# Kernel tuning notes

Hardware: AMD Instinct MI355X
Metric: run time of the kernel (lower is better)

Reference implementation:

```python
import jax, jax.numpy as jnp
import numpy as np
import math

D_MODEL = 64
H = 8
DK = D_MODEL // H


def setup_inputs() -> dict:
    key = jax.random.key(0)
    ks = jax.random.split(key, 6)
    B, C, T, N = 8, D_MODEL, 12, 307
    x = jax.random.normal(ks[0], (B, C, T, N), dtype=jnp.float32)
    mask = jax.random.randint(ks[1], (B, N, N), 0, 2, dtype=jnp.int32)
    s = 1.0 / math.sqrt(D_MODEL)
    Wq = jax.random.uniform(ks[2], (D_MODEL, D_MODEL), jnp.float32, -s, s)
    bq = jax.random.uniform(ks[3], (D_MODEL,), jnp.float32, -s, s)
    Wk = jax.random.uniform(ks[4], (D_MODEL, D_MODEL), jnp.float32, -s, s)
    bk = jax.random.uniform(ks[5], (D_MODEL,), jnp.float32, -s, s)
    return {"x": x, "mask": mask, "Wq": Wq, "bq": bq, "Wk": Wk, "bk": bk}


def reference(x, mask, Wq, bq, Wk, bk):
    # x: [B, d_model, T, N] -> [B, T, N, d_model]
    B, C, T, N = x.shape
    xp = jnp.transpose(x, (0, 2, 3, 1))
    # torch Linear: y = x W^T + b
    q = jnp.einsum('btnd,ed->btne', xp, Wq) + bq
    k = jnp.einsum('btnd,ed->btne', xp, Wk) + bk
    # split heads: [B, T, N, h, dk]
    q = q.reshape(B, T, N, H, DK)
    k = k.reshape(B, T, N, H, DK)
    # QK^T per head then sum over heads (einsum 'ijkmn->ijmn'), fused:
    # scores: [B, T, N, N]
    scores = jnp.einsum('btnhd,btmhd->btnm', q, k) / math.sqrt(DK)
    # mask.unsqueeze(1) -> [B, 1, N, N]
    scores = jnp.where(mask[:, None] == 0, jnp.float32(-1e9), scores)
    # softmax over last dim; dropout is identity in eval mode
    return jax.nn.softmax(scores, axis=-1)
```

## Files before the change

### kernel.cpp

```cpp
#include <hip/hip_runtime.h>
#include <math.h>

#define PB 8
#define PT 12
#define PN 307
#define NP 320
#define SCALE 0.35355339059327373f

typedef short bf16x8 __attribute__((ext_vector_type(8)));
typedef float f32x4  __attribute__((ext_vector_type(4)));
typedef int   i32x4u __attribute__((ext_vector_type(4), aligned(4)));
typedef float f32x4u __attribute__((ext_vector_type(4), aligned(4)));

__device__ __forceinline__ unsigned short f32_to_bf16(float v) {
    unsigned u = __float_as_uint(v);
    u += 0x7FFFu + ((u >> 16) & 1u);
    return (unsigned short)(u >> 16);
}

__device__ __forceinline__ bf16x8 pack8(float4 lo, float4 hi) {
    bf16x8 r;
    r[0] = (short)f32_to_bf16(lo.x); r[1] = (short)f32_to_bf16(lo.y);
    r[2] = (short)f32_to_bf16(lo.z); r[3] = (short)f32_to_bf16(lo.w);
    r[4] = (short)f32_to_bf16(hi.x); r[5] = (short)f32_to_bf16(hi.y);
    r[6] = (short)f32_to_bf16(hi.z); r[7] = (short)f32_to_bf16(hi.w);
    return r;
}

__global__ __launch_bounds__(256) void qk_proj_kernel(
    const float* __restrict__ x,
    const float* __restrict__ Wq, const float* __restrict__ bq,
    const float* __restrict__ Wk, const float* __restrict__ bk,
    unsigned short* __restrict__ qws, unsigned short* __restrict__ kws)
{
    const int tid  = threadIdx.x;
    const int lane = tid & 63;
    const int wv   = tid >> 6;
    const int wn   = wv & 1;
    const int we   = wv >> 1;
    const int chunk = blockIdx.x % 10;
    const int bt    = blockIdx.x / 10;
    const int b = bt / PT, t = bt % PT;
    const int rlo = lane & 15;
    const int kq  = lane >> 4;
    const int n0  = chunk * 32 + wn * 16;

    const int nn = min(n0 + rlo, PN - 1);
    const float* xrow = x + ((size_t)b * 64 * PT + t) * PN + nn;
    bf16x8 a[2];
    #pragma unroll
    for (int ks = 0; ks < 2; ++ks) {
        #pragma unroll
        for (int j = 0; j < 8; ++j) {
            const int c = ks * 32 + kq * 8 + j;
            a[ks][j] = (short)f32_to_bf16(xrow[(size_t)c * PT * PN]);
        }
    }

    f32x4 accq[2] = {}, acck[2] = {};
    #pragma unroll
    for (int eti = 0; eti < 2; ++eti) {
        const int e_row = we * 32 + eti * 16 + rlo;
        const float* wq_r = Wq + (size_t)e_row * 64 + kq * 8;
        const float* wk_r = Wk + (size_t)e_row * 64 + kq * 8;
        #pragma unroll
        for (int ks = 0; ks < 2; ++ks) {
            const bf16x8 bqf = pack8(*(const float4*)(wq_r + ks * 32),
                                     *(const float4*)(wq_r + ks * 32 + 4));
            const bf16x8 bkf = pack8(*(const float4*)(wk_r + ks * 32),
                                     *(const float4*)(wk_r + ks * 32 + 4));
            accq[eti] = __builtin_amdgcn_mfma_f32_16x16x32_bf16(a[ks], bqf, accq[eti], 0, 0, 0);
            acck[eti] = __builtin_amdgcn_mfma_f32_16x16x32_bf16(a[ks], bkf, acck[eti], 0, 0, 0);
        }
    }

    #pragma unroll
    for (int eti = 0; eti < 2; ++eti) {
        const int e = we * 32 + eti * 16 + rlo;
        const float bqv = bq[e], bkv = bk[e];
        #pragma unroll
        for (int r = 0; r < 4; ++r) {
            const int n = n0 + kq * 4 + r;
            if (n < PN) {
                qws[((size_t)bt * NP + n) * 64 + e] = f32_to_bf16(accq[eti][r] + bqv);
                kws[((size_t)bt * NP + n) * 64 + e] = f32_to_bf16(acck[eti][r] + bkv);
            }
        }
    }
}

__global__ __launch_bounds__(256) void attn_kernel(
    const unsigned short* __restrict__ qws,
    const unsigned short* __restrict__ kws,
    const int* __restrict__ mask,
    float* __restrict__ out)
{
    __shared__ float redmx[4][16];
    __shared__ float redsm[4][16];

    const int tid  = threadIdx.x;
    const int lane = tid & 63;
    const int wm   = tid >> 6;
    const int ntile = blockIdx.x % 20;
    const int bt    = blockIdx.x / 20;
    const int b     = bt / PT;
    const int ng  = ntile * 16;
    const int nl  = lane & 15;
    const int kq  = lane >> 4;
    const int n   = ng + nl;
    const int nn  = (n < PN) ? n : (PN - 1);

    const bf16x8* qp = (const bf16x8*)(qws + ((size_t)bt * NP + n) * 64 + kq * 8);
    const bf16x8 bq0 = qp[0], bq1 = qp[4];
    const unsigned short* kbase = kws + ((size_t)bt * NP + nl) * 64 + kq * 8;

    f32x4 acc[5] = {};
    #pragma unroll
    for (int i = 0; i < 5; ++i) {
        const int ct = wm * 5 + i;
        const unsigned short* kb = kbase + (size_t)ct * 16 * 64;
        const bf16x8 a0 = *(const bf16x8*)(kb);
        const bf16x8 a1 = *(const bf16x8*)(kb + 32);
        acc[i] = __builtin_amdgcn_mfma_f32_16x16x32_bf16(a0, bq0, acc[i], 0, 0, 0);
        acc[i] = __builtin_amdgcn_mfma_f32_16x16x32_bf16(a1, bq1, acc[i], 0, 0, 0);
    }

    const int* mrow = mask + ((size_t)b * PN + nn) * PN;
    float mx = -INFINITY;
    #pragma unroll
    for (int i = 0; i < 5; ++i) {
        const int ct = wm * 5 + i;
        const int m0 = ct * 16 + kq * 4;
        const i32x4u mv = *(const i32x4u*)(mrow + m0);
        float sv[4];
        sv[0] = mv[0] ? acc[i][0] * SCALE : -1e9f;
        sv[1] = mv[1] ? acc[i][1] * SCALE : -1e9f;
        sv[2] = mv[2] ? acc[i][2] * SCALE : -1e9f;
        sv[3] = mv[3] ? acc[i][3] * SCALE : -1e9f;
        if (ct == 19) {
            #pragma unroll
            for (int r = 0; r < 4; ++r)
                if (m0 + r >= PN) sv[r] = -INFINITY;
        }
        #pragma unroll
        for (int r = 0; r < 4; ++r) { acc[i][r] = sv[r]; mx = fmaxf(mx, sv[r]); }
    }
    mx = fmaxf(mx, __shfl_xor(mx, 16));
    mx = fmaxf(mx, __shfl_xor(mx, 32));
    if (lane < 16) redmx[wm][lane] = mx;
    __syncthreads();
    const float gmx = fmaxf(fmaxf(redmx[0][nl], redmx[1][nl]),
                            fmaxf(redmx[2][nl], redmx[3][nl]));

    float sum = 0.f;
    #pragma unroll
    for (int i = 0; i < 5; ++i) {
        #pragma unroll
        for (int r = 0; r < 4; ++r) {
            const float p = __expf(acc[i][r] - gmx);
            acc[i][r] = p;
            sum += p;
        }
    }
    sum += __shfl_xor(sum, 16);
    sum += __shfl_xor(sum, 32);
    if (lane < 16) redsm[wm][lane] = sum;
    __syncthreads();
    const float inv = 1.0f / (redsm[0][nl] + redsm[1][nl] +
                              redsm[2][nl] + redsm[3][nl]);

    if (n < PN) {
        float* orow = out + ((size_t)bt * PN + n) * PN;
        #pragma unroll
        for (int i = 0; i < 5; ++i) {
            const int ct = wm * 5 + i;
            const int m0 = ct * 16 + kq * 4;
            if (ct < 19) {
                f32x4u o;
                o[0] = acc[i][0] * inv; o[1] = acc[i][1] * inv;
                o[2] = acc[i][2] * inv; o[3] = acc[i][3] * inv;
                *(f32x4u*)(orow + m0) = o;
            } else {
                #pragma unroll
                for (int r = 0; r < 4; ++r)
                    if (m0 + r < PN) orow[m0 + r] = acc[i][r] * inv;
            }
        }
    }
}

extern "C" void kernel_launch(void* const* d_in, const int* in_sizes, int n_in,
                              void* d_out, int out_size, void* d_ws, size_t ws_size,
                              hipStream_t stream) {
    const float* x  = (const float*)d_in[0];
    const int* mask = (const int*)d_in[1];
    const float* Wq = (const float*)d_in[2];
    const float* bq = (const float*)d_in[3];
    const float* Wk = (const float*)d_in[4];
    const float* bk = (const float*)d_in[5];
    float* out = (float*)d_out;

    unsigned short* qws = (unsigned short*)d_ws;
    unsigned short* kws = qws + (size_t)96 * NP * 64;

    qk_proj_kernel<<<dim3(96 * 10), dim3(256), 0, stream>>>(x, Wq, bq, Wk, bk, qws, kws);
    attn_kernel<<<dim3(96 * 20), dim3(256), 0, stream>>>(qws, kws, mask, out);
}
```

Baseline: 107.7 us.

## Reuse mask loads across four time steps per attention block

Each attention block now handles four consecutive time steps of one batch. It loads its mask slice into registers once and loops over t, instead of reloading the mask for every (b,t) block. The reduction buffers are double-buffered by time-step parity so the loop needs no extra barrier. This cuts repeated mask reads from global memory, but the grid shrinks from 1920 to 480 blocks, which lowers parallelism and the latency hiding that came from many blocks in flight.

Measured after the change: 104.2 us. -3.2%, faster.

```diff
diff --git a/kernel.cpp b/kernel.cpp
--- a/kernel.cpp
+++ b/kernel.cpp
@@ -95,95 +95,108 @@
     const int* __restrict__ mask,
     float* __restrict__ out)
 {
-    __shared__ float redmx[4][16];
-    __shared__ float redsm[4][16];
+    __shared__ float redmx[2][4][16];
+    __shared__ float redsm[2][4][16];
 
     const int tid  = threadIdx.x;
     const int lane = tid & 63;
     const int wm   = tid >> 6;
-    const int ntile = blockIdx.x % 20;
-    const int bt    = blockIdx.x / 20;
-    const int b     = bt / PT;
+    const int bid   = blockIdx.x;
+    const int ntile = bid % 20;
+    const int r2    = bid / 20;
+    const int tg    = r2 % 3;
+    const int b     = r2 / 3;
     const int ng  = ntile * 16;
     const int nl  = lane & 15;
     const int kq  = lane >> 4;
     const int n   = ng + nl;
     const int nn  = (n < PN) ? n : (PN - 1);
 
-    const bf16x8* qp = (const bf16x8*)(qws + ((size_t)bt * NP + n) * 64 + kq * 8);
-    const bf16x8 bq0 = qp[0], bq1 = qp[4];
-    const unsigned short* kbase = kws + ((size_t)bt * NP + nl) * 64 + kq * 8;
-
-    f32x4 acc[5] = {};
-    #pragma unroll
-    for (int i = 0; i < 5; ++i) {
-        const int ct = wm * 5 + i;
-        const unsigned short* kb = kbase + (size_t)ct * 16 * 64;
-        const bf16x8 a0 = *(const bf16x8*)(kb);
-        const bf16x8 a1 = *(const bf16x8*)(kb + 32);
-        acc[i] = __builtin_amdgcn_mfma_f32_16x16x32_bf16(a0, bq0, acc[i], 0, 0, 0);
-        acc[i] = __builtin_amdgcn_mfma_f32_16x16x32_bf16(a1, bq1, acc[i], 0, 0, 0);
-    }
-
     const int* mrow = mask + ((size_t)b * PN + nn) * PN;
-    float mx = -INFINITY;
-    #pragma unroll
-    for (int i = 0; i < 5; ++i) {
-        const int ct = wm * 5 + i;
-        const int m0 = ct * 16 + kq * 4;
-        const i32x4u mv = *(const i32x4u*)(mrow + m0);
-        float sv[4];
-        sv[0] = mv[0] ? acc[i][0] * SCALE : -1e9f;
-        sv[1] = mv[1] ? acc[i][1] * SCALE : -1e9f;
-        sv[2] = mv[2] ? acc[i][2] * SCALE : -1e9f;
-        sv[3] = mv[3] ? acc[i][3] * SCALE : -1e9f;
-        if (ct == 19) {
-            #pragma unroll
-            for (int r = 0; r < 4; ++r)
-                if (m0 + r >= PN) sv[r] = -INFINITY;
-        }
-        #pragma unroll
-        for (int r = 0; r < 4; ++r) { acc[i][r] = sv[r]; mx = fmaxf(mx, sv[r]); }
-    }
-    mx = fmaxf(mx, __shfl_xor(mx, 16));
-    mx = fmaxf(mx, __shfl_xor(mx, 32));
-    if (lane < 16) redmx[wm][lane] = mx;
-    __syncthreads();
-    const float gmx = fmaxf(fmaxf(redmx[0][nl], redmx[1][nl]),
-                            fmaxf(redmx[2][nl], redmx[3][nl]));
-
-    float sum = 0.f;
-    #pragma unroll
-    for (int i = 0; i < 5; ++i) {
-        #pragma unroll
-        for (int r = 0; r < 4; ++r) {
-            const float p = __expf(acc[i][r] - gmx);
-            acc[i][r] = p;
-            sum += p;
-        }
-    }
-    sum += __shfl_xor(sum, 16);
-    sum += __shfl_xor(sum, 32);
-    if (lane < 16) redsm[wm][lane] = sum;
-    __syncthreads();
-    const float inv = 1.0f / (redsm[0][nl] + redsm[1][nl] +
-                              redsm[2][nl] + redsm[3][nl]);
-
-    if (n < PN) {
-        float* orow = out + ((size_t)bt * PN + n) * PN;
+    i32x4u mv[5];
+    #pragma unroll
+    for (int i = 0; i < 5; ++i)
+        mv[i] = *(const i32x4u*)(mrow + (wm * 5 + i) * 16 + kq * 4);
+
+    #pragma unroll 1
+    for (int tt = 0; tt < 4; ++tt) {
+        const int t  = tg * 4 + tt;
+        const int bt = b * PT + t;
+        const int p  = tt & 1;
+
+        const bf16x8* qp = (const bf16x8*)(qws + ((size_t)bt * NP + n) * 64 + kq * 8);
+        const bf16x8 bq0 = qp[0], bq1 = qp[4];
+        const unsigned short* kbase = kws + ((size_t)bt * NP + nl) * 64 + kq * 8;
+
+        f32x4 acc[5] = {};
+        #pragma unroll
+        for (int i = 0; i < 5; ++i) {
+            const int ct = wm * 5 + i;
+            const unsigned short* kb = kbase + (size_t)ct * 16 * 64;
+            const bf16x8 a0 = *(const bf16x8*)(kb);
+            const bf16x8 a1 = *(const bf16x8*)(kb + 32);
+            acc[i] = __builtin_amdgcn_mfma_f32_16x16x32_bf16(a0, bq0, acc[i], 0, 0, 0);
+            acc[i] = __builtin_amdgcn_mfma_f32_16x16x32_bf16(a1, bq1, acc[i], 0, 0, 0);
+        }
+
+        float mx = -INFINITY;
         #pragma unroll
         for (int i = 0; i < 5; ++i) {
             const int ct = wm * 5 + i;
             const int m0 = ct * 16 + kq * 4;
-            if (ct < 19) {
-                f32x4u o;
-                o[0] = acc[i][0] * inv; o[1] = acc[i][1] * inv;
-                o[2] = acc[i][2] * inv; o[3] = acc[i][3] * inv;
-                *(f32x4u*)(orow + m0) = o;
-            } else {
+            float sv[4];
+            sv[0] = mv[i][0] ? acc[i][0] * SCALE : -1e9f;
+            sv[1] = mv[i][1] ? acc[i][1] * SCALE : -1e9f;
+            sv[2] = mv[i][2] ? acc[i][2] * SCALE : -1e9f;
+            sv[3] = mv[i][3] ? acc[i][3] * SCALE : -1e9f;
+            if (ct == 19) {
                 #pragma unroll
                 for (int r = 0; r < 4; ++r)
-                    if (m0 + r < PN) orow[m0 + r] = acc[i][r] * inv;
+                    if (m0 + r >= PN) sv[r] = -INFINITY;
+            }
+            #pragma unroll
+            for (int r = 0; r < 4; ++r) { acc[i][r] = sv[r]; mx = fmaxf(mx, sv[r]); }
+        }
+        mx = fmaxf(mx, __shfl_xor(mx, 16));
+        mx = fmaxf(mx, __shfl_xor(mx, 32));
+        if (lane < 16) redmx[p][wm][lane] = mx;
+        __syncthreads();
+        const float gmx = fmaxf(fmaxf(redmx[p][0][nl], redmx[p][1][nl]),
+                                fmaxf(redmx[p][2][nl], redmx[p][3][nl]));
+
+        float sum = 0.f;
+        #pragma unroll
+        for (int i = 0; i < 5; ++i) {
+            #pragma unroll
+            for (int r = 0; r < 4; ++r) {
+                const float pw = __expf(acc[i][r] - gmx);
+                acc[i][r] = pw;
+                sum += pw;
+            }
+        }
+        sum += __shfl_xor(sum, 16);
+        sum += __shfl_xor(sum, 32);
+        if (lane < 16) redsm[p][wm][lane] = sum;
+        __syncthreads();
+        const float inv = 1.0f / (redsm[p][0][nl] + redsm[p][1][nl] +
+                                  redsm[p][2][nl] + redsm[p][3][nl]);
+
+        if (n < PN) {
+            float* orow = out + ((size_t)bt * PN + n) * PN;
+            #pragma unroll
+            for (int i = 0; i < 5; ++i) {
+                const int ct = wm * 5 + i;
+                const int m0 = ct * 16 + kq * 4;
+                if (ct < 19) {
+                    f32x4u o;
+                    o[0] = acc[i][0] * inv; o[1] = acc[i][1] * inv;
+                    o[2] = acc[i][2] * inv; o[3] = acc[i][3] * inv;
+                    *(f32x4u*)(orow + m0) = o;
+                } else {
+                    #pragma unroll
+                    for (int r = 0; r < 4; ++r)
+                        if (m0 + r < PN) orow[m0 + r] = acc[i][r] * inv;
+                }
             }
         }
     }
@@ -204,5 +217,5 @@
     unsigned short* kws = qws + (size_t)96 * NP * 64;
 
     qk_proj_kernel<<<dim3(96 * 10), dim3(256), 0, stream>>>(x, Wq, bq, Wk, bk, qws, kws);
-    attn_kernel<<<dim3(96 * 20), dim3(256), 0, stream>>>(qws, kws, mask, out);
-}
+    attn_kernel<<<dim3(8 * 3 * 20), dim3(256), 0, stream>>>(qws, kws, mask, out);
+}
```
